# Optimization experiments

Hardware: AMD Instinct MI355X
Metric: run time of the kernel (lower is better)

The kernel has to match this reference:

```python
import jax, jax.numpy as jnp
import numpy as np
from jax import lax

B, L, V, H = 2, 1024, 32000, 1024
EXP = 2; INNER = H * EXP; S = 16; DT = 64; K = 4
F_FFN = 2048; E = 8; TOPK = 2; EPS = 1e-5


def setup_inputs() -> dict:
    key = jax.random.key(0)
    ks = jax.random.split(key, 12)
    def nrm(k, shape, s=0.02):
        return jax.random.normal(k, shape, jnp.float32) * s
    inp = {}
    inp["input_ids"] = jax.random.randint(ks[0], (B, L), 0, V)
    inp["emb"] = nrm(ks[1], (V, H))
    inp["norm0_w"] = jnp.ones((H,), jnp.float32)
    inp["in_proj_w"] = nrm(ks[2], (2 * INNER, H))
    inp["conv_w"] = nrm(ks[3], (INNER, 1, K), 0.1)
    inp["conv_b"] = jnp.zeros((INNER,), jnp.float32)
    inp["x_proj_w"] = nrm(ks[4], (DT + 2 * S, INNER))
    inp["dt_proj_w"] = nrm(ks[5], (INNER, DT), 0.05)
    inp["dt_proj_b"] = jnp.full((INNER,), -2.0, jnp.float32)
    inp["a_log"] = jnp.log(jnp.broadcast_to(jnp.arange(1, S + 1, dtype=jnp.float32), (INNER, S)))
    inp["d_param"] = jnp.ones((INNER,), jnp.float32)
    inp["out_proj_w"] = nrm(ks[6], (H, INNER))
    inp["norm1_w"] = jnp.ones((H,), jnp.float32)
    inp["router_w"] = nrm(ks[7], (E, H))
    inp["router_b"] = jnp.zeros((E,), jnp.float32)
    inp["fc1_w"] = nrm(ks[8], (E, 2 * F_FFN, H))
    inp["fc2_w"] = nrm(ks[9], (E, H, F_FFN))
    inp["final_norm_w"] = jnp.ones((H,), jnp.float32)
    return inp


def _rms(x, w):
    return (x * lax.rsqrt(jnp.mean(x * x, -1, keepdims=True) + EPS)) * w


def _mamba_scan(u, delta, a_log, b, c, d):
    # u, delta: [B,L,INNER]; b, c: [B,L,S]; a_log: [INNER,S]; d: [INNER]
    a = -jnp.exp(a_log)
    dl = jax.nn.softplus(delta)
    def step(st, inp):
        u_t, d_t, b_t, c_t = inp  # [B,INNER], [B,INNER], [B,S], [B,S]
        st = jnp.exp(d_t[:, :, None] * a[None]) * st + (d_t * u_t)[:, :, None] * b_t[:, None, :]
        y = jnp.sum(st * c_t[:, None, :], -1) + u_t * d
        return st, y
    st0 = jnp.zeros((u.shape[0], INNER, S), jnp.float32)
    tm = lambda x: jnp.swapaxes(x, 0, 1)  # time-major
    _, ys = lax.scan(step, st0, (tm(u), tm(dl), tm(b), tm(c)))
    return tm(ys)


def reference(input_ids, emb, norm0_w, in_proj_w, conv_w, conv_b, x_proj_w,
              dt_proj_w, dt_proj_b, a_log, d_param, out_proj_w, norm1_w,
              router_w, router_b, fc1_w, fc2_w, final_norm_w):
    x = emb[input_ids]  # [B,L,H]
    # ---- layer 0: Mamba mixer ----
    xn = _rms(x, norm0_w)
    proj = xn @ in_proj_w.T  # [B,L,2*INNER]
    u, gate = proj[..., :INNER], proj[..., INNER:]
    u_t = jnp.swapaxes(u, 1, 2)  # [B,INNER,L]
    uc = lax.conv_general_dilated(u_t, conv_w, (1,), [(K - 1, 0)],
                                  dimension_numbers=('NCH', 'OIH', 'NCH'),
                                  feature_group_count=INNER) + conv_b[None, :, None]
    u_conv = jax.nn.silu(jnp.swapaxes(uc, 1, 2))  # [B,L,INNER]
    xp = u_conv @ x_proj_w.T  # [B,L,DT+2S]
    dt, b, c = xp[..., :DT], xp[..., DT:DT + S], xp[..., DT + S:]
    delta = dt @ dt_proj_w.T + dt_proj_b
    y = _mamba_scan(u_conv, delta, a_log, b, c, d_param)
    x = x + (y * jax.nn.silu(gate)) @ out_proj_w.T
    # ---- layer 1: dense MoE (every expert over all tokens, as reference) ----
    xn = _rms(x, norm1_w)
    logits = xn @ router_w.T + router_b  # [B,L,E]
    probs = jax.nn.softmax(logits, -1)
    topk_s, topk_i = lax.top_k(probs, TOPK)
    scores = jnp.sum(jax.nn.one_hot(topk_i, E, dtype=x.dtype) * topk_s[..., None], axis=2)  # [B,L,E]
    h1 = jnp.einsum('blh,eoh->belo', xn, fc1_w)  # [B,E,L,2F]
    hidden = jax.nn.silu(h1[..., :F_FFN]) * h1[..., F_FFN:]
    eo = jnp.einsum('belf,ehf->belh', hidden, fc2_w)  # [B,E,L,H]
    x = x + jnp.einsum('belh,ble->blh', eo, scores)
    # ---- final norm + tied lm head ----
    x = _rms(x, final_norm_w)
    return x @ emb.T  # [B,L,V]
```

## Files before the change

### kernel.cpp

```cpp
#include <hip/hip_runtime.h>
#include <cstdint>

#define HD 1024
#define INNER 2048
#define NTOK 2048
#define SEQL 1024
#define SDIM 16
#define DTR 64
#define VDIM 32000
#define FFN 2048
#define EPSV 1e-5f
#define SLOT_CAP 5120
#define MAX_TILES 40
#define NCH 32
#define CLEN 32

typedef __attribute__((ext_vector_type(8))) short short8;
typedef __attribute__((ext_vector_type(4))) float f32x4;

__device__ __forceinline__ unsigned short f2bf(float f){
  unsigned int u = __float_as_uint(f);
  u += 0x7FFF + ((u >> 16) & 1);
  return (unsigned short)(u >> 16);
}
__device__ __forceinline__ float sigm(float x){ return 1.f/(1.f+__expf(-x)); }

__device__ __forceinline__ void gload16(const unsigned short* g, unsigned short* l){
  __builtin_amdgcn_global_load_lds(
    (const __attribute__((address_space(1))) unsigned int*)g,
    (__attribute__((address_space(3))) unsigned int*)l, 16, 0, 0);
}

__device__ __forceinline__ float block_sum(float v, float* sb){
  #pragma unroll
  for (int m=32;m>=1;m>>=1) v += __shfl_xor(v, m, 64);
  int lane = threadIdx.x & 63, w = threadIdx.x >> 6;
  if (lane==0) sb[w]=v;
  __syncthreads();
  float s = sb[0]+sb[1]+sb[2]+sb[3];
  __syncthreads();
  return s;
}

__global__ __launch_bounds__(256) void embed_rms_k(
  const int* __restrict__ ids, const float* __restrict__ emb,
  const float* __restrict__ n0w, float* __restrict__ x, float* __restrict__ xn)
{
  __shared__ float sb[4];
  int tok = blockIdx.x, t = threadIdx.x;
  int id = ids[tok];
  float4 v = *(const float4*)(emb + (size_t)id*HD + t*4);
  *(float4*)(x + (size_t)tok*HD + t*4) = v;
  float tot = block_sum(v.x*v.x+v.y*v.y+v.z*v.z+v.w*v.w, sb);
  float rs = rsqrtf(tot/(float)HD + EPSV);
  float4 w = *(const float4*)(n0w + t*4);
  float4 o; o.x=v.x*rs*w.x; o.y=v.y*rs*w.y; o.z=v.z*rs*w.z; o.w=v.w*rs*w.w;
  *(float4*)(xn + (size_t)tok*HD + t*4) = o;
}

template<int EPI>
__global__ __launch_bounds__(256) void gemm_f32k(
  const float* __restrict__ A, int lda,
  const float* __restrict__ B,
  float* __restrict__ C, int ldc,
  int N, int K, const float* __restrict__ bias)
{
  __shared__ float As[16][68];
  __shared__ float Bs[16][68];
  int m0 = blockIdx.y*64, n0 = blockIdx.x*64;
  int t = threadIdx.x, tm = t & 15, tn = t >> 4;
  float acc[4][4] = {};
  int srow = t >> 2, skq = (t & 3) * 4;
  const float* arow = A + (size_t)(m0 + srow)*lda + skq;
  int nrow = n0 + srow;
  const float* brow = B + (size_t)nrow*K + skq;
  bool bok = nrow < N;
  for (int k0 = 0; k0 < K; k0 += 16) {
    float4 a = *(const float4*)(arow + k0);
    float4 b = bok ? *(const float4*)(brow + k0) : make_float4(0.f,0.f,0.f,0.f);
    __syncthreads();
    As[skq+0][srow]=a.x; As[skq+1][srow]=a.y; As[skq+2][srow]=a.z; As[skq+3][srow]=a.w;
    Bs[skq+0][srow]=b.x; Bs[skq+1][srow]=b.y; Bs[skq+2][srow]=b.z; Bs[skq+3][srow]=b.w;
    __syncthreads();
    #pragma unroll
    for (int k=0;k<16;k++){
      const float4 av = *(const float4*)&As[k][tm*4];
      const float4 bv = *(const float4*)&Bs[k][tn*4];
      float am[4] = {av.x, av.y, av.z, av.w};
      float bn[4] = {bv.x, bv.y, bv.z, bv.w};
      #pragma unroll
      for (int i=0;i<4;i++)
        #pragma unroll
        for (int j=0;j<4;j++)
          acc[i][j] += am[i]*bn[j];
    }
  }
  #pragma unroll
  for (int i=0;i<4;i++){
    int row = m0 + tm*4 + i;
    #pragma unroll
    for (int j=0;j<4;j++){
      int col = n0 + tn*4 + j;
      if (col < N){
        float v = acc[i][j];
        if (EPI==1){ v += bias[col]; v = (v > 20.f) ? v : log1pf(expf(v)); }
        if (EPI==2){ v += C[(size_t)row*ldc + col]; }
        C[(size_t)row*ldc + col] = v;
      }
    }
  }
}

__global__ __launch_bounds__(256) void conv_silu_k(
  const float* __restrict__ proj, const float* __restrict__ cw,
  const float* __restrict__ cb, float* __restrict__ uc)
{
  int idx = blockIdx.x*256 + threadIdx.x;
  int c = idx & (INNER-1);
  int l = (idx >> 11) & (SEQL-1);
  int b = idx >> 21;
  float s = cb[c];
  #pragma unroll
  for (int k=0;k<4;k++){
    int ll = l + k - 3;
    if (ll >= 0) s += proj[(size_t)(b*SEQL + ll)*4096 + c] * cw[c*4+k];
  }
  uc[idx] = s * sigm(s);
}

__global__ __launch_bounds__(256) void scan_p1(
  const float* __restrict__ dl, const float* __restrict__ uc,
  const float* __restrict__ xp, const float* __restrict__ alog,
  float* __restrict__ locfin, float* __restrict__ Pst)
{
  int c = blockIdx.x*256 + threadIdx.x;
  int chunk = blockIdx.y, b = blockIdx.z;
  float a[SDIM];
  #pragma unroll
  for (int s=0;s<SDIM;s++) a[s] = -expf(alog[c*SDIM+s]);
  float st[SDIM] = {};
  float P[SDIM];
  #pragma unroll
  for (int s=0;s<SDIM;s++) P[s] = 1.f;
  size_t base = (size_t)b*SEQL + chunk*CLEN;
  #pragma unroll 2
  for (int l=0;l<CLEN;l++){
    size_t tix = base + l;
    float d = dl[tix*INNER + c];
    float u = uc[tix*INNER + c];
    const float* bc = xp + tix*96 + 64;
    float w = d*u;
    #pragma unroll
    for (int s=0;s<SDIM;s++){
      float p = __expf(d*a[s]);
      st[s] = p*st[s] + w*bc[s];
      P[s] *= p;
    }
  }
  size_t cb = (size_t)(b*NCH + chunk)*SDIM*INNER + c;
  #pragma unroll
  for (int s=0;s<SDIM;s++){
    locfin[cb + (size_t)s*INNER] = st[s];
    Pst[cb + (size_t)s*INNER] = P[s];
  }
}

__global__ __launch_bounds__(256) void scan_p2(
  const float* __restrict__ locfin, const float* __restrict__ Pst,
  float* __restrict__ initst)
{
  int c = blockIdx.x*256 + threadIdx.x;
  int s = blockIdx.y, b = blockIdx.z;
  float carry = 0.f;
  #pragma unroll 4
  for (int chunk=0; chunk<NCH; chunk++){
    size_t idx = ((size_t)(b*NCH + chunk)*SDIM + s)*INNER + c;
    initst[idx] = carry;
    carry = Pst[idx]*carry + locfin[idx];
  }
}

__global__ __launch_bounds__(256) void scan_p3(
  const float* __restrict__ dl, const float* __restrict__ uc,
  const float* __restrict__ xp, const float* __restrict__ alog,
  const float* __restrict__ dpar, const float* __restrict__ initst,
  float* __restrict__ y)
{
  int c = blockIdx.x*256 + threadIdx.x;
  int chunk = blockIdx.y, b = blockIdx.z;
  float a[SDIM], st[SDIM];
  #pragma unroll
  for (int s=0;s<SDIM;s++) a[s] = -expf(alog[c*SDIM+s]);
  size_t cb = (size_t)(b*NCH + chunk)*SDIM*INNER + c;
  #pragma unroll
  for (int s=0;s<SDIM;s++) st[s] = initst[cb + (size_t)s*INNER];
  float dv = dpar[c];
  size_t base = (size_t)b*SEQL + chunk*CLEN;
  #pragma unroll 2
  for (int l=0;l<CLEN;l++){
    size_t tix = base + l;
    float d = dl[tix*INNER + c];
    float u = uc[tix*INNER + c];
    const float* bc = xp + tix*96 + 64;
    float w = d*u, acc = 0.f;
    #pragma unroll
    for (int s=0;s<SDIM;s++){
      float p = __expf(d*a[s]);
      st[s] = p*st[s] + w*bc[s];
      acc += st[s]*bc[16+s];
    }
    y[tix*INNER + c] = acc + u*dv;
  }
}

__global__ __launch_bounds__(256) void ygate_k(
  const float* __restrict__ y, const float* __restrict__ proj, float* __restrict__ yg)
{
  int idx = blockIdx.x*256 + threadIdx.x;
  int c = idx & (INNER-1); int t_ = idx >> 11;
  float g = proj[(size_t)t_*4096 + 2048 + c];
  yg[idx] = y[idx] * g * sigm(g);
}

__global__ __launch_bounds__(256) void rms_router_k(
  const float* __restrict__ x, const float* __restrict__ n1w,
  const float* __restrict__ rw, const float* __restrict__ rb,
  unsigned short* __restrict__ xnbf, int* __restrict__ ti, float* __restrict__ ts)
{
  __shared__ float sb[4];
  __shared__ float sb8[8][4];
  int tok = blockIdx.x, t = threadIdx.x;
  float4 v = *(const float4*)(x + (size_t)tok*HD + t*4);
  float tot = block_sum(v.x*v.x+v.y*v.y+v.z*v.z+v.w*v.w, sb);
  float rs = rsqrtf(tot/(float)HD + EPSV);
  float4 w = *(const float4*)(n1w + t*4);
  float4 xv; xv.x=v.x*rs*w.x; xv.y=v.y*rs*w.y; xv.z=v.z*rs*w.z; xv.w=v.w*rs*w.w;
  ushort4 o; o.x=f2bf(xv.x); o.y=f2bf(xv.y); o.z=f2bf(xv.z); o.w=f2bf(xv.w);
  *(ushort4*)(xnbf + (size_t)tok*HD + t*4) = o;
  float pe[8];
  #pragma unroll
  for (int e=0;e<8;e++){
    const float4 r4 = *(const float4*)(rw + (size_t)e*HD + t*4);
    pe[e] = xv.x*r4.x + xv.y*r4.y + xv.z*r4.z + xv.w*r4.w;
  }
  int lane = t & 63, wv = t >> 6;
  #pragma unroll
  for (int e=0;e<8;e++){
    float s = pe[e];
    #pragma unroll
    for (int m=32;m>=1;m>>=1) s += __shfl_xor(s, m, 64);
    if (lane==0) sb8[e][wv] = s;
  }
  __syncthreads();
  if (t==0){
    float lg[8], mx = -1e30f;
    for (int e=0;e<8;e++){ lg[e] = sb8[e][0]+sb8[e][1]+sb8[e][2]+sb8[e][3] + rb[e]; mx = fmaxf(mx, lg[e]); }
    float ex[8], sum=0.f;
    for (int e=0;e<8;e++){ ex[e]=expf(lg[e]-mx); sum+=ex[e]; }
    float inv = 1.f/sum;
    int i0=0; float p0=-1.f;
    for (int e=0;e<8;e++){ float p=ex[e]*inv; if (p>p0){p0=p;i0=e;} }
    int i1=-1; float p1=-1.f;
    for (int e=0;e<8;e++){ if (e==i0) continue; float p=ex[e]*inv; if (p>p1){p1=p;i1=e;} }
    ti[2*tok]=i0; ti[2*tok+1]=i1; ts[2*tok]=p0; ts[2*tok+1]=p1;
  }
}

__global__ void route_build_k(const int* __restrict__ ti, const float* __restrict__ ts,
  int* __restrict__ slot_token, int* __restrict__ tok_slots, int* __restrict__ tile_expert)
{
  __shared__ int cnt[8], cur[8];
  int t = threadIdx.x;
  if (t < 8) cnt[t] = 0;
  __syncthreads();
  for (int tok = t; tok < NTOK; tok += 256){
    atomicAdd(&cnt[ti[2*tok]], 1);
    atomicAdd(&cnt[ti[2*tok+1]], 1);
  }
  __syncthreads();
  if (t == 0){
    int off = 0, tile = 0;
    for (int e=0;e<8;e++){
      cur[e] = off;
      int nt2 = (cnt[e] + 127) >> 7;
      for (int j=0;j<nt2;j++) tile_expert[tile++] = e;
      off += nt2 << 7;
    }
    while (tile < MAX_TILES) tile_expert[tile++] = -1;
  }
  __syncthreads();
  for (int i = t; i < SLOT_CAP; i += 256) slot_token[i] = -1;
  __syncthreads();
  for (int tok = t; tok < NTOK; tok += 256){
    #pragma unroll
    for (int j=0;j<2;j++){
      int e = ti[2*tok+j];
      int p = atomicAdd(&cur[e], 1);
      slot_token[p] = tok;
      tok_slots[2*tok+j] = p;
    }
  }
}

template<bool GATHER, bool EXPERT>
__global__ __launch_bounds__(256) void gemm_bf16k(
  const unsigned short* __restrict__ A, int lda,
  const int* __restrict__ slot_token,
  const float* __restrict__ B0, long long expert_stride,
  const int* __restrict__ tile_expert,
  float* __restrict__ C, int ldc, int K)
{
  int mt = blockIdx.y, nt = blockIdx.x;
  const float* Bp = B0;
  if (EXPERT){
    int e = tile_expert[mt];
    if (e < 0) return;
    Bp = B0 + (long long)e * expert_stride;
  }
  int m0 = mt*128, n0 = nt*128;
  __shared__ unsigned short As[128][40];
  __shared__ unsigned short Bs[128][40];
  int t = threadIdx.x;
  int w = t >> 6, lane = t & 63;
  int wm = (w >> 1) * 64, wn = (w & 1) * 64;
  int lr = lane & 15, quad = lane >> 4;
  f32x4 acc[4][4] = {};

  int arow = t >> 1;
  int ahalf = t & 1;
  const unsigned short* asrc = nullptr;
  bool avalid = true;
  if (GATHER){
    int tok = slot_token[m0 + arow];
    avalid = (tok >= 0);
    if (avalid) asrc = A + (size_t)tok * lda;
  } else {
    asrc = A + (size_t)(m0 + arow) * lda;
  }
  const float* bsrc = Bp + (size_t)(n0 + arow) * K;

  for (int k0 = 0; k0 < K; k0 += 32){
    uint4 av0 = make_uint4(0,0,0,0), av1 = make_uint4(0,0,0,0);
    if (avalid){
      const uint4* p = (const uint4*)(asrc + k0 + ahalf*16);
      av0 = p[0]; av1 = p[1];
    }
    const float4* q = (const float4*)(bsrc + k0 + ahalf*16);
    float4 b0 = q[0], b1 = q[1], b2 = q[2], b3 = q[3];
    uint4 w0, w1;
    w0.x = (uint32_t)f2bf(b0.x) | ((uint32_t)f2bf(b0.y)<<16);
    w0.y = (uint32_t)f2bf(b0.z) | ((uint32_t)f2bf(b0.w)<<16);
    w0.z = (uint32_t)f2bf(b1.x) | ((uint32_t)f2bf(b1.y)<<16);
    w0.w = (uint32_t)f2bf(b1.z) | ((uint32_t)f2bf(b1.w)<<16);
    w1.x = (uint32_t)f2bf(b2.x) | ((uint32_t)f2bf(b2.y)<<16);
    w1.y = (uint32_t)f2bf(b2.z) | ((uint32_t)f2bf(b2.w)<<16);
    w1.z = (uint32_t)f2bf(b3.x) | ((uint32_t)f2bf(b3.y)<<16);
    w1.w = (uint32_t)f2bf(b3.z) | ((uint32_t)f2bf(b3.w)<<16);
    __syncthreads();
    *(uint4*)&As[arow][ahalf*16]     = av0;
    *(uint4*)&As[arow][ahalf*16 + 8] = av1;
    *(uint4*)&Bs[arow][ahalf*16]     = w0;
    *(uint4*)&Bs[arow][ahalf*16 + 8] = w1;
    __syncthreads();
    short8 af[4], bf[4];
    #pragma unroll
    for (int mi=0;mi<4;mi++) af[mi] = *(const short8*)&As[wm + mi*16 + lr][quad*8];
    #pragma unroll
    for (int ni=0;ni<4;ni++) bf[ni] = *(const short8*)&Bs[wn + ni*16 + lr][quad*8];
    #pragma unroll
    for (int mi=0;mi<4;mi++)
      #pragma unroll
      for (int ni=0;ni<4;ni++)
        acc[mi][ni] = __builtin_amdgcn_mfma_f32_16x16x32_bf16(af[mi], bf[ni], acc[mi][ni], 0, 0, 0);
  }
  #pragma unroll
  for (int mi=0;mi<4;mi++){
    int rbase = m0 + wm + mi*16 + quad*4;
    #pragma unroll
    for (int ni=0;ni<4;ni++){
      int col = n0 + wn + ni*16 + lr;
      float* cp = C + (size_t)rbase*ldc + col;
      #pragma unroll
      for (int r=0;r<4;r++) cp[(size_t)r*ldc] = acc[mi][ni][r];
    }
  }
}

__global__ __launch_bounds__(256) void f2bf_arr_k(
  const float* __restrict__ in, unsigned short* __restrict__ out)
{
  size_t i = (size_t)(blockIdx.x*256 + threadIdx.x) * 8;
  const float4* p = (const float4*)(in + i);
  float4 a = p[0], b = p[1];
  ushort4 o0, o1;
  o0.x=f2bf(a.x); o0.y=f2bf(a.y); o0.z=f2bf(a.z); o0.w=f2bf(a.w);
  o1.x=f2bf(b.x); o1.y=f2bf(b.y); o1.z=f2bf(b.z); o1.w=f2bf(b.w);
  *(ushort4*)(out + i)     = o0;
  *(ushort4*)(out + i + 4) = o1;
}

__global__ __launch_bounds__(256) void lmhead_k(
  const unsigned short* __restrict__ A,
  const unsigned short* __restrict__ B,
  float* __restrict__ C)
{
  __shared__ __align__(16) unsigned short As[128][32];
  __shared__ __align__(16) unsigned short Bs[128][32];
  int orig = blockIdx.x;
  int swz = (orig & 7)*500 + (orig >> 3);
  int mt = swz & 15, nt = swz >> 4;
  int m0 = mt*128, n0 = nt*128;
  int t = threadIdx.x, w = t >> 6, lane = t & 63;
  int wm = (w >> 1) * 64, wn = (w & 1) * 64;
  int lr = lane & 15, quad = lane >> 4;

  int o0 = w*1024 + lane*16;
  int o1 = o0 + 4096;
  const unsigned short* gA0 = A + (size_t)(m0 + (o0>>6))*HD + ((o0&63)>>1);
  const unsigned short* gA1 = A + (size_t)(m0 + (o1>>6))*HD + ((o1&63)>>1);
  const unsigned short* gB0 = B + (size_t)(n0 + (o0>>6))*HD + ((o0&63)>>1);
  const unsigned short* gB1 = B + (size_t)(n0 + (o1>>6))*HD + ((o1&63)>>1);
  unsigned short* dA0 = &As[0][0] + (o0>>1);
  unsigned short* dA1 = &As[0][0] + (o1>>1);
  unsigned short* dB0 = &Bs[0][0] + (o0>>1);
  unsigned short* dB1 = &Bs[0][0] + (o1>>1);

  f32x4 acc[4][4] = {};
  for (int k0 = 0; k0 < HD; k0 += 32){
    __syncthreads();
    gload16(gA0 + k0, dA0);
    gload16(gA1 + k0, dA1);
    gload16(gB0 + k0, dB0);
    gload16(gB1 + k0, dB1);
    __syncthreads();
    short8 af[4], bf[4];
    #pragma unroll
    for (int mi=0;mi<4;mi++) af[mi] = *(const short8*)&As[wm + mi*16 + lr][quad*8];
    #pragma unroll
    for (int ni=0;ni<4;ni++) bf[ni] = *(const short8*)&Bs[wn + ni*16 + lr][quad*8];
    #pragma unroll
    for (int mi=0;mi<4;mi++)
      #pragma unroll
      for (int ni=0;ni<4;ni++)
        acc[mi][ni] = __builtin_amdgcn_mfma_f32_16x16x32_bf16(af[mi], bf[ni], acc[mi][ni], 0, 0, 0);
  }
  #pragma unroll
  for (int mi=0;mi<4;mi++){
    int rbase = m0 + wm + mi*16 + quad*4;
    #pragma unroll
    for (int ni=0;ni<4;ni++){
      int col = n0 + wn + ni*16 + lr;
      float* cp = C + (size_t)rbase*VDIM + col;
      #pragma unroll
      for (int r=0;r<4;r++) cp[(size_t)r*VDIM] = acc[mi][ni][r];
    }
  }
}

__global__ __launch_bounds__(256) void silu_mul_k(
  const float* __restrict__ h1, unsigned short* __restrict__ hidden)
{
  int idx = blockIdx.x*256 + threadIdx.x;
  int f = idx & (FFN-1); int slot = idx >> 11;
  float a = h1[(size_t)slot*2*FFN + f];
  float b = h1[(size_t)slot*2*FFN + FFN + f];
  hidden[idx] = f2bf(a*sigm(a)*b);
}

__global__ __launch_bounds__(256) void combine_rms_k(
  const float* __restrict__ x, const float* __restrict__ eo,
  const int* __restrict__ tok_slots, const float* __restrict__ ts,
  const float* __restrict__ fw, unsigned short* __restrict__ xnf)
{
  __shared__ float sb[4];
  int tok = blockIdx.x, t = threadIdx.x;
  int p0 = tok_slots[2*tok], p1 = tok_slots[2*tok+1];
  float s0 = ts[2*tok], s1 = ts[2*tok+1];
  float4 v  = *(const float4*)(x  + (size_t)tok*HD + t*4);
  float4 e0 = *(const float4*)(eo + (size_t)p0*HD + t*4);
  float4 e1 = *(const float4*)(eo + (size_t)p1*HD + t*4);
  v.x += s0*e0.x + s1*e1.x;
  v.y += s0*e0.y + s1*e1.y;
  v.z += s0*e0.z + s1*e1.z;
  v.w += s0*e0.w + s1*e1.w;
  float tot = block_sum(v.x*v.x+v.y*v.y+v.z*v.z+v.w*v.w, sb);
  float rs = rsqrtf(tot/(float)HD + EPSV);
  float4 w = *(const float4*)(fw + t*4);
  ushort4 o;
  o.x=f2bf(v.x*rs*w.x); o.y=f2bf(v.y*rs*w.y); o.z=f2bf(v.z*rs*w.z); o.w=f2bf(v.w*rs*w.w);
  *(ushort4*)(xnf + (size_t)tok*HD + t*4) = o;
}

extern "C" void kernel_launch(void* const* d_in, const int* in_sizes, int n_in,
                              void* d_out, int out_size, void* d_ws, size_t ws_size,
                              hipStream_t stream)
{
  const int*   ids  = (const int*)  d_in[0];
  const float* emb  = (const float*)d_in[1];
  const float* n0w  = (const float*)d_in[2];
  const float* ipw  = (const float*)d_in[3];
  const float* cw   = (const float*)d_in[4];
  const float* cb   = (const float*)d_in[5];
  const float* xpw  = (const float*)d_in[6];
  const float* dtw  = (const float*)d_in[7];
  const float* dtb  = (const float*)d_in[8];
  const float* alog = (const float*)d_in[9];
  const float* dpar = (const float*)d_in[10];
  const float* opw  = (const float*)d_in[11];
  const float* n1w  = (const float*)d_in[12];
  const float* rw   = (const float*)d_in[13];
  const float* rb   = (const float*)d_in[14];
  const float* f1w  = (const float*)d_in[15];
  const float* f2w  = (const float*)d_in[16];
  const float* fnw  = (const float*)d_in[17];
  float* out = (float*)d_out;
  char* ws = (char*)d_ws;

  size_t o_x       = 0;
  size_t o_xnbf    = o_x + 8388608;
  size_t o_ti      = o_xnbf + 4194304;
  size_t o_ts      = o_ti + 16384;
  size_t o_slott   = o_ts + 16384;
  size_t o_tslots  = o_slott + 20480;
  size_t o_tile    = o_tslots + 16384;
  size_t o_xn      = o_tile + 256;
  size_t o_proj    = o_xn + 8388608;
  size_t o_uconv   = o_proj + 33554432;
  size_t o_xp      = o_uconv + 16777216;
  size_t o_dl      = o_xp + 786432;
  size_t o_y       = o_dl + 16777216;
  size_t o_yg      = o_y + 16777216;
  size_t o_h1      = o_proj;
  size_t o_hidden  = o_yg + 16777216;
  size_t o_eo      = o_hidden + 20971520;
  size_t o_xnf     = o_eo + 20971520;
  size_t o_locfin  = o_hidden;
  size_t o_pst     = o_locfin + 8388608;
  size_t o_init    = o_pst + 8388608;
  size_t o_embbf   = o_proj;

  float* x      = (float*)(ws + o_x);
  unsigned short* xnbf = (unsigned short*)(ws + o_xnbf);
  int*   ti     = (int*)(ws + o_ti);
  float* ts     = (float*)(ws + o_ts);
  int*   slott  = (int*)(ws + o_slott);
  int*   tslots = (int*)(ws + o_tslots);
  int*   tile_e = (int*)(ws + o_tile);
  float* xn     = (float*)(ws + o_xn);
  float* proj   = (float*)(ws + o_proj);
  float* uconv  = (float*)(ws + o_uconv);
  float* xp     = (float*)(ws + o_xp);
  float* dl     = (float*)(ws + o_dl);
  float* y      = (float*)(ws + o_y);
  float* yg     = (float*)(ws + o_yg);
  float* h1     = (float*)(ws + o_h1);
  unsigned short* hidden = (unsigned short*)(ws + o_hidden);
  float* eo     = (float*)(ws + o_eo);
  unsigned short* xnf = (unsigned short*)(ws + o_xnf);
  float* locfin = (float*)(ws + o_locfin);
  float* pst    = (float*)(ws + o_pst);
  float* initst = (float*)(ws + o_init);
  unsigned short* embbf = (unsigned short*)(ws + o_embbf);

  embed_rms_k<<<NTOK,256,0,stream>>>(ids, emb, n0w, x, xn);
  gemm_f32k<0><<<dim3(64,32),256,0,stream>>>(xn, HD, ipw, proj, 4096, 4096, HD, nullptr);
  conv_silu_k<<<(NTOK*INNER)/256,256,0,stream>>>(proj, cw, cb, uconv);
  gemm_f32k<0><<<dim3(2,32),256,0,stream>>>(uconv, INNER, xpw, xp, 96, 96, INNER, nullptr);
  gemm_f32k<1><<<dim3(32,32),256,0,stream>>>(xp, 96, dtw, dl, INNER, INNER, DTR, dtb);
  scan_p1<<<dim3(8,NCH,2),256,0,stream>>>(dl, uconv, xp, alog, locfin, pst);
  scan_p2<<<dim3(8,SDIM,2),256,0,stream>>>(locfin, pst, initst);
  scan_p3<<<dim3(8,NCH,2),256,0,stream>>>(dl, uconv, xp, alog, dpar, initst, y);
  ygate_k<<<(NTOK*INNER)/256,256,0,stream>>>(y, proj, yg);
  gemm_f32k<2><<<dim3(16,32),256,0,stream>>>(yg, INNER, opw, x, HD, HD, INNER, nullptr);
  rms_router_k<<<NTOK,256,0,stream>>>(x, n1w, rw, rb, xnbf, ti, ts);
  route_build_k<<<1,256,0,stream>>>(ti, ts, slott, tslots, tile_e);
  gemm_bf16k<true,true><<<dim3(32,MAX_TILES),256,0,stream>>>(
      xnbf, HD, slott, f1w, 4096LL*1024LL, tile_e, h1, 4096, HD);
  silu_mul_k<<<(SLOT_CAP*FFN)/256,256,0,stream>>>(h1, hidden);
  f2bf_arr_k<<<(VDIM*HD/8)/256,256,0,stream>>>(emb, embbf);
  gemm_bf16k<false,true><<<dim3(8,MAX_TILES),256,0,stream>>>(
      hidden, FFN, nullptr, f2w, 1024LL*2048LL, tile_e, eo, HD, FFN);
  combine_rms_k<<<NTOK,256,0,stream>>>(x, eo, tslots, ts, fnw, xnf);
  lmhead_k<<<4000,256,0,stream>>>(xnf, embbf, out);
}
```

Measured before the change: 1.519 ms.

## Double-buffer LM-head GEMM shared tiles and XOR-swizzle LDS layout

Switches the LM-head bf16 MFMA GEMM from one shared-memory buffer to two alternating buffers. The next K-slice's global-to-LDS loads are issued before computing on the current slice, and one barrier is dropped per iteration. It also XOR-swizzles the column offset within each 32-element LDS row on both the load and read sides to reduce bank conflicts. This doubles shared-memory use per block, which may lower occupancy, and the swizzle must match exactly between writes and reads.

```diff
diff --git a/kernel.cpp b/kernel.cpp
--- a/kernel.cpp
+++ b/kernel.cpp
@@ -404,8 +404,10 @@
   const unsigned short* __restrict__ B,
   float* __restrict__ C)
 {
-  __shared__ __align__(16) unsigned short As[128][32];
-  __shared__ __align__(16) unsigned short Bs[128][32];
+  __shared__ __align__(16) unsigned short As0[128][32];
+  __shared__ __align__(16) unsigned short Bs0[128][32];
+  __shared__ __align__(16) unsigned short As1[128][32];
+  __shared__ __align__(16) unsigned short Bs1[128][32];
   int orig = blockIdx.x;
   int swz = (orig & 7)*500 + (orig >> 3);
   int mt = swz & 15, nt = swz >> 4;
@@ -414,36 +416,50 @@
   int wm = (w >> 1) * 64, wn = (w & 1) * 64;
   int lr = lane & 15, quad = lane >> 4;
 
-  int o0 = w*1024 + lane*16;
-  int o1 = o0 + 4096;
-  const unsigned short* gA0 = A + (size_t)(m0 + (o0>>6))*HD + ((o0&63)>>1);
-  const unsigned short* gA1 = A + (size_t)(m0 + (o1>>6))*HD + ((o1&63)>>1);
-  const unsigned short* gB0 = B + (size_t)(n0 + (o0>>6))*HD + ((o0&63)>>1);
-  const unsigned short* gB1 = B + (size_t)(n0 + (o1>>6))*HD + ((o1&63)>>1);
-  unsigned short* dA0 = &As[0][0] + (o0>>1);
-  unsigned short* dA1 = &As[0][0] + (o1>>1);
-  unsigned short* dB0 = &Bs[0][0] + (o0>>1);
-  unsigned short* dB1 = &Bs[0][0] + (o1>>1);
+  int row0 = w*16 + (lane>>2);
+  int koff = ((lane&3) ^ ((lane>>3)&3)) * 8;
+  int p0 = (w*1024 + lane*16) >> 1;
+  int p1 = p0 + 2048;
+  const unsigned short* gA0 = A + (size_t)(m0 + row0)*HD + koff;
+  const unsigned short* gA1 = gA0 + (size_t)64*HD;
+  const unsigned short* gB0 = B + (size_t)(n0 + row0)*HD + koff;
+  const unsigned short* gB1 = gB0 + (size_t)64*HD;
+
+  int sq = (quad ^ ((lr>>1)&3)) * 8;
 
   f32x4 acc[4][4] = {};
-  for (int k0 = 0; k0 < HD; k0 += 32){
+
+#define STAGE(AS,BS,k0) \
+    gload16(gA0 + (k0), &AS[0][0] + p0); \
+    gload16(gA1 + (k0), &AS[0][0] + p1); \
+    gload16(gB0 + (k0), &BS[0][0] + p0); \
+    gload16(gB1 + (k0), &BS[0][0] + p1);
+
+#define COMPUTE(AS,BS) { \
+    short8 af[4], bf[4]; \
+    _Pragma("unroll") \
+    for (int mi=0;mi<4;mi++) af[mi] = *(const short8*)&AS[wm + mi*16 + lr][sq]; \
+    _Pragma("unroll") \
+    for (int ni=0;ni<4;ni++) bf[ni] = *(const short8*)&BS[wn + ni*16 + lr][sq]; \
+    _Pragma("unroll") \
+    for (int mi=0;mi<4;mi++) \
+      _Pragma("unroll") \
+      for (int ni=0;ni<4;ni++) \
+        acc[mi][ni] = __builtin_amdgcn_mfma_f32_16x16x32_bf16(af[mi], bf[ni], acc[mi][ni], 0, 0, 0); }
+
+  STAGE(As0,Bs0, 0);
+  __syncthreads();
+  for (int k0 = 0; k0 < HD; k0 += 64){
+    STAGE(As1,Bs1, k0+32);
+    COMPUTE(As0,Bs0);
     __syncthreads();
-    gload16(gA0 + k0, dA0);
-    gload16(gA1 + k0, dA1);
-    gload16(gB0 + k0, dB0);
-    gload16(gB1 + k0, dB1);
+    if (k0 + 64 < HD) { STAGE(As0,Bs0, k0+64); }
+    COMPUTE(As1,Bs1);
     __syncthreads();
-    short8 af[4], bf[4];
-    #pragma unroll
-    for (int mi=0;mi<4;mi++) af[mi] = *(const short8*)&As[wm + mi*16 + lr][quad*8];
-    #pragma unroll
-    for (int ni=0;ni<4;ni++) bf[ni] = *(const short8*)&Bs[wn + ni*16 + lr][quad*8];
-    #pragma unroll
-    for (int mi=0;mi<4;mi++)
-      #pragma unroll
-      for (int ni=0;ni<4;ni++)
-        acc[mi][ni] = __builtin_amdgcn_mfma_f32_16x16x32_bf16(af[mi], bf[ni], acc[mi][ni], 0, 0, 0);
-  }
+  }
+#undef STAGE
+#undef COMPUTE
+
   #pragma unroll
   for (int mi=0;mi<4;mi++){
     int rbase = m0 + wm + mi*16 + quad*4;
```

Result: faster. 1.428 ms (-6.0%).
